# Kernel optimization log

Measured on AMD Instinct MI355X. Metric: run time of the kernel, lower is better.

Reference implementation:

```python
import jax, jax.numpy as jnp
import numpy as np

SHIFT = 1  # module picks random.random()>0.5 -> +/-1; fixed to +1 for determinism


def setup_inputs() -> dict:
    key = jax.random.key(0)
    k1, k2 = jax.random.split(key)
    x = jax.random.normal(k1, (1, 128, 14, 14), dtype=jnp.float32)
    w = jax.random.normal(k2, (32, 3, 128), dtype=jnp.float32)  # [out_c, kernel, in_c]
    return {"x": x, "w": w}


def reference(x, w):
    # roll + reshape + unfold + permute + einsum chain is equivalent to:
    #   circular roll along W, 1D conv along W (k=3, zero pad 1, 128->32, per H row),
    #   circular roll along H.
    xr = jnp.roll(x, SHIFT, axis=3)
    # w[j,k,i] -> OIHW kernel (32, 128, 1, 3); H kernel size 1, W kernel size 3
    kern = jnp.transpose(w, (0, 2, 1))[:, :, None, :]
    y = jax.lax.conv_general_dilated(
        xr, kern,
        window_strides=(1, 1),
        padding=((0, 0), (1, 1)),
        dimension_numbers=("NCHW", "OIHW", "NCHW"),
    )  # (1, 32, 14, 14)
    return jnp.roll(y, SHIFT, axis=2)
```

## Files before the change

kernel.cpp:

```cpp
#include <hip/hip_runtime.h>


__global__ __launch_bounds__(256) void conv_roll_kernel(
    const float* __restrict__ x,
    const float* __restrict__ wt,
    float* __restrict__ out)
{
    __shared__ float red[224];

    const int bx = blockIdx.x;
    const int o  = bx / 14;
    const int h  = bx - o * 14;
    const int hh = (h + 13) % 14;
    const int rb = hh * 14;

    const int t = threadIdx.x;

    if (t < 224) {
        const int ci = t / 14;
        const int w  = t - ci * 14;

        const int c0 = rb + ((w + 12) % 14);
        const int c1 = rb + ((w + 13) % 14);
        const int c2 = rb + w;

        const float* __restrict__ wo = wt + o * 384 + ci * 8;
        const float* __restrict__ xb = x + (ci * 8) * 196;

        float a0 = 0.f, a1 = 0.f, a2 = 0.f;
#pragma unroll
        for (int j = 0; j < 8; ++j) {
            const float* __restrict__ xp = xb + j * 196;
            a0 = __builtin_fmaf(xp[c0], wo[j],       a0);
            a1 = __builtin_fmaf(xp[c1], wo[128 + j], a1);
            a2 = __builtin_fmaf(xp[c2], wo[256 + j], a2);
        }

        const float m0 = (w > 0)  ? 1.0f : 0.0f;
        const float m2 = (w < 13) ? 1.0f : 0.0f;
        red[t] = m0 * a0 + a1 + m2 * a2;
    }

    __syncthreads();

    if (t < 14) {
        float s = 0.f;
#pragma unroll
        for (int ci = 0; ci < 16; ++ci)
            s += red[ci * 14 + t];
        out[o * 196 + h * 14 + t] = s;
    }
}

extern "C" void kernel_launch(void* const* d_in, const int* in_sizes, int n_in,
                              void* d_out, int out_size, void* d_ws, size_t ws_size,
                              hipStream_t stream) {
    const float* x  = (const float*)d_in[0];
    const float* wt = (const float*)d_in[1];
    float* out = (float*)d_out;

    conv_roll_kernel<<<448, 256, 0, stream>>>(x, wt, out);
}
```

Measured before the change: 56.58 us.

## Split each output across 16 lanes and reduce with shuffles instead of LDS

Each group of 16 threads now computes one output element, with each lane covering 8 input channels. Lanes combine partial sums with xor shuffles, which removes the shared-memory buffer, the block barrier and the serial 14-thread reduction. Weights are fetched as float4 vector loads. The grid changes to 392 fully used blocks, where the old layout left 32 of 256 threads idle in every block. In exchange, x values are reloaded redundantly across groups and the number of gather loads per thread stays the same.

```diff
diff --git a/kernel.cpp b/kernel.cpp
--- a/kernel.cpp
+++ b/kernel.cpp
@@ -6,50 +6,50 @@
     const float* __restrict__ wt,
     float* __restrict__ out)
 {
-    __shared__ float red[224];
+    const int t = threadIdx.x;
+    const int g = t >> 4;
+    const int r = t & 15;
 
-    const int bx = blockIdx.x;
-    const int o  = bx / 14;
-    const int h  = bx - o * 14;
-    const int hh = (h + 13) % 14;
-    const int rb = hh * 14;
+    const int oid = (blockIdx.x << 4) + g;
+    const int o   = oid / 196;
+    const int rem = oid - o * 196;
+    const int h   = rem / 14;
+    const int w   = rem - h * 14;
 
-    const int t = threadIdx.x;
+    const int rb = ((h + 13) % 14) * 14;
+    const int c0 = rb + ((w + 12) % 14);
+    const int c1 = rb + ((w + 13) % 14);
+    const int c2 = rb + w;
 
-    if (t < 224) {
-        const int ci = t / 14;
-        const int w  = t - ci * 14;
+    const float* __restrict__ wo = wt + o * 384 + r * 8;
+    float wv[3][8];
+    *reinterpret_cast<float4*>(&wv[0][0]) = *reinterpret_cast<const float4*>(wo);
+    *reinterpret_cast<float4*>(&wv[0][4]) = *reinterpret_cast<const float4*>(wo + 4);
+    *reinterpret_cast<float4*>(&wv[1][0]) = *reinterpret_cast<const float4*>(wo + 128);
+    *reinterpret_cast<float4*>(&wv[1][4]) = *reinterpret_cast<const float4*>(wo + 132);
+    *reinterpret_cast<float4*>(&wv[2][0]) = *reinterpret_cast<const float4*>(wo + 256);
+    *reinterpret_cast<float4*>(&wv[2][4]) = *reinterpret_cast<const float4*>(wo + 260);
 
-        const int c0 = rb + ((w + 12) % 14);
-        const int c1 = rb + ((w + 13) % 14);
-        const int c2 = rb + w;
+    const float* __restrict__ xb = x + (r * 8) * 196;
 
-        const float* __restrict__ wo = wt + o * 384 + ci * 8;
-        const float* __restrict__ xb = x + (ci * 8) * 196;
-
-        float a0 = 0.f, a1 = 0.f, a2 = 0.f;
+    float a0 = 0.f, a1 = 0.f, a2 = 0.f;
 #pragma unroll
-        for (int j = 0; j < 8; ++j) {
-            const float* __restrict__ xp = xb + j * 196;
-            a0 = __builtin_fmaf(xp[c0], wo[j],       a0);
-            a1 = __builtin_fmaf(xp[c1], wo[128 + j], a1);
-            a2 = __builtin_fmaf(xp[c2], wo[256 + j], a2);
-        }
-
-        const float m0 = (w > 0)  ? 1.0f : 0.0f;
-        const float m2 = (w < 13) ? 1.0f : 0.0f;
-        red[t] = m0 * a0 + a1 + m2 * a2;
+    for (int j = 0; j < 8; ++j) {
+        const float* __restrict__ xp = xb + j * 196;
+        a0 = __builtin_fmaf(xp[c0], wv[0][j], a0);
+        a1 = __builtin_fmaf(xp[c1], wv[1][j], a1);
+        a2 = __builtin_fmaf(xp[c2], wv[2][j], a2);
     }
 
-    __syncthreads();
+    float s = a1 + ((w > 0)  ? a0 : 0.f)
+                 + ((w < 13) ? a2 : 0.f);
 
-    if (t < 14) {
-        float s = 0.f;
-#pragma unroll
-        for (int ci = 0; ci < 16; ++ci)
-            s += red[ci * 14 + t];
-        out[o * 196 + h * 14 + t] = s;
-    }
+    s += __shfl_xor(s, 1);
+    s += __shfl_xor(s, 2);
+    s += __shfl_xor(s, 4);
+    s += __shfl_xor(s, 8);
+
+    if (r == 0) out[oid] = s;
 }
 
 extern "C" void kernel_launch(void* const* d_in, const int* in_sizes, int n_in,
@@ -59,5 +59,5 @@
     const float* wt = (const float*)d_in[1];
     float* out = (float*)d_out;
 
-    conv_roll_kernel<<<448, 256, 0, stream>>>(x, wt, out);
+    conv_roll_kernel<<<392, 256, 0, stream>>>(x, wt, out);
 }
```

After: 60.22 us. 1.06x slower.
